# Kernel optimization log

Measured on AMD Instinct MI355X. Metric: run time of the kernel, lower is better.

Reference implementation:

```python
import jax, jax.numpy as jnp
import numpy as np

B, N, D = 2, 2048, 1024
H, HD = 16, 64


def setup_inputs() -> dict:
    key = jax.random.key(0)
    ks = jax.random.split(key, 5)
    return {
        "hidden_states": jax.random.normal(ks[0], (B, N, D), dtype=jnp.float32),
        "W_attn": jax.random.normal(ks[1], (D, 3 * D), dtype=jnp.float32) * (D ** -0.5),
        "b_attn": jax.random.normal(ks[2], (3 * D,), dtype=jnp.float32) * 0.02,
        "W_proj": jax.random.normal(ks[3], (D, D), dtype=jnp.float32) * (D ** -0.5),
        "b_proj": jax.random.normal(ks[4], (D,), dtype=jnp.float32) * 0.02,
    }


def reference(hidden_states, W_attn, b_attn, W_proj, b_proj):
    # QKV projection: [B,N,3D]
    proj = hidden_states @ W_attn + b_attn
    q, k, v = jnp.split(proj, 3, axis=-1)
    # [B,N,H,HD]
    q = q.reshape(B, N, H, HD)
    k = k.reshape(B, N, H, HD)
    v = v.reshape(B, N, H, HD)
    scale = HD ** -0.5
    # naive attention: full [B,H,Nq,Nkv] score matrix
    attn = jnp.einsum("bqhd,bkhd->bhqk", q, k) * scale
    q_pos = jnp.arange(N)
    kv_pos = jnp.arange(N)
    # mask where kv_pos > start_pos + q_pos (start_pos = 0)
    mask = kv_pos[None, :] > q_pos[:, None]  # [Nq, Nkv]
    attn = jnp.where(mask[None, None, :, :], -jnp.inf, attn)
    attn = jax.nn.softmax(attn, axis=-1)
    out = jnp.einsum("bhqk,bkhd->bqhd", attn, v)  # [B,N,H,HD]
    out = out.reshape(B, N, D)
    return out @ W_proj + b_proj
```

## Files before the change

kernel.cpp:

```cpp
#include <hip/hip_runtime.h>
#include <hip/hip_bf16.h>

#define BB 2
#define NN 2048
#define DDIM 1024
#define HH 16
#define HDD 64

typedef __attribute__((ext_vector_type(8))) short bf16x8;
typedef __attribute__((ext_vector_type(4))) short bf16x4;
typedef __attribute__((ext_vector_type(4))) float f32x4;

__device__ inline ushort f2bf(float x) {
  __hip_bfloat16 h = __float2bfloat16(x);
  ushort u;
  __builtin_memcpy(&u, &h, 2);
  return u;
}
__device__ inline float bf2f(ushort u) {
  unsigned v = (unsigned)u << 16;
  float f;
  __builtin_memcpy(&f, &v, 4);
  return f;
}
__device__ inline float exp2_raw(float x) {
  float r;
  asm("v_exp_f32 %0, %1" : "=v"(r) : "v"(x));
  return r;
}

#define GLOAD_LDS16(g, l)                                                              \
  __builtin_amdgcn_global_load_lds((const __attribute__((address_space(1))) void*)(g), \
                                   (__attribute__((address_space(3))) void*)(l), 16, 0, 0)

__global__ __launch_bounds__(256) void cvt_f32_bf16(const float* __restrict__ in,
                                                    ushort* __restrict__ out, int n4) {
  int i = blockIdx.x * 256 + threadIdx.x;
  if (i >= n4) return;
  float4 a = ((const float4*)in)[i];
  ushort4 o;
  o.x = f2bf(a.x); o.y = f2bf(a.y); o.z = f2bf(a.z); o.w = f2bf(a.w);
  ((ushort4*)out)[i] = o;
}

__global__ __launch_bounds__(256) void transpose_cvt(const float* __restrict__ in,
                                                     ushort* __restrict__ out, int R, int C) {
  __shared__ float tile[32][33];
  int bx = blockIdx.x * 32, by = blockIdx.y * 32;
  int tx = threadIdx.x, ty = threadIdx.y;
#pragma unroll
  for (int r = ty; r < 32; r += 8)
    tile[r][tx] = in[(size_t)(by + r) * C + bx + tx];
  __syncthreads();
#pragma unroll
  for (int r = ty; r < 32; r += 8)
    out[(size_t)(bx + r) * R + by + tx] = f2bf(tile[tx][r]);
}

template <int MODE>
__global__ __launch_bounds__(256) void gemm_bt(const ushort* __restrict__ A,
                                               const ushort* __restrict__ Bt,
                                               const float* __restrict__ bias,
                                               void* __restrict__ Cv,
                                               ushort* __restrict__ Vt,
                                               int M, int N, int K) {
  __shared__ ushort As[128 * 32];
  __shared__ ushort Bs[128 * 32];
  const int tid = threadIdx.x;
  const int wid = tid >> 6, lane = tid & 63;
  const int c = lane & 15, g = lane >> 4;
  const int wm = (wid >> 1) * 64, wn = (wid & 1) * 64;
  const int m0 = blockIdx.y * 128, n0 = blockIdx.x * 128;
  f32x4 acc[4][4] = {};
  for (int k0 = 0; k0 < K; k0 += 32) {
    __syncthreads();
#pragma unroll
    for (int it = 0; it < 2; ++it) {
      int G = tid + it * 256;
      int row = G >> 2, sl = G & 3;
      GLOAD_LDS16(A + (size_t)(m0 + row) * K + k0 + sl * 8, &As[G * 8]);
      GLOAD_LDS16(Bt + (size_t)(n0 + row) * K + k0 + sl * 8, &Bs[G * 8]);
    }
    __syncthreads();
    bf16x8 af[4], bfr[4];
#pragma unroll
    for (int i = 0; i < 4; ++i) {
      af[i] = *(const bf16x8*)(&As[(wm + i * 16 + c) * 32 + g * 8]);
      bfr[i] = *(const bf16x8*)(&Bs[(wn + i * 16 + c) * 32 + g * 8]);
    }
#pragma unroll
    for (int i = 0; i < 4; ++i)
#pragma unroll
      for (int j = 0; j < 4; ++j)
        acc[i][j] = __builtin_amdgcn_mfma_f32_16x16x32_bf16(af[i], bfr[j], acc[i][j], 0, 0, 0);
  }
#pragma unroll
  for (int i = 0; i < 4; ++i) {
#pragma unroll
    for (int j = 0; j < 4; ++j) {
      const int col = n0 + wn + j * 16 + c;
      const float bv = bias[col];
      const int row = m0 + wm + i * 16 + g * 4;
      if (MODE == 2 && col >= 2048) {
        const int hh = (col - 2048) >> 6, dd = (col - 2048) & 63;
        const int bb = row >> 11, nl = row & 2047;
        ushort4 ov;
        ov.x = f2bf(acc[i][j][0] + bv);
        ov.y = f2bf(acc[i][j][1] + bv);
        ov.z = f2bf(acc[i][j][2] + bv);
        ov.w = f2bf(acc[i][j][3] + bv);
        *(ushort4*)(&Vt[(size_t)((bb * 16 + hh) * 64 + dd) * NN + nl]) = ov;
      } else {
        const int ldc = (MODE == 2) ? 2048 : N;
#pragma unroll
        for (int ri = 0; ri < 4; ++ri) {
          float v = acc[i][j][ri] + bv;
          ((ushort*)Cv)[(size_t)(row + ri) * ldc + col] = f2bf(v);
        }
      }
    }
  }
}

__global__ __launch_bounds__(256) void gemm_proj(const ushort* __restrict__ A,
                                                 const ushort* __restrict__ Bt,
                                                 const float* __restrict__ bias,
                                                 float* __restrict__ C, int M, int N, int K) {
  __shared__ ushort As[64 * 32];
  __shared__ ushort Bs[128 * 32];
  const int tid = threadIdx.x;
  const int wid = tid >> 6, lane = tid & 63;
  const int c = lane & 15, g = lane >> 4;
  const int wn = wid * 32;
  const int m0 = blockIdx.y * 64, n0 = blockIdx.x * 128;
  f32x4 acc[4][2] = {};
  for (int k0 = 0; k0 < K; k0 += 32) {
    __syncthreads();
#pragma unroll
    for (int it = 0; it < 3; ++it) {
      int G = tid + it * 256;
      if (G < 256) {
        int row = G >> 2, sl = G & 3;
        GLOAD_LDS16(A + (size_t)(m0 + row) * K + k0 + sl * 8, &As[G * 8]);
      } else {
        int GB = G - 256;
        int row = GB >> 2, sl = GB & 3;
        GLOAD_LDS16(Bt + (size_t)(n0 + row) * K + k0 + sl * 8, &Bs[GB * 8]);
      }
    }
    __syncthreads();
    bf16x8 af[4], bfr[2];
#pragma unroll
    for (int i = 0; i < 4; ++i) af[i] = *(const bf16x8*)(&As[(i * 16 + c) * 32 + g * 8]);
#pragma unroll
    for (int j = 0; j < 2; ++j)
      bfr[j] = *(const bf16x8*)(&Bs[(wn + j * 16 + c) * 32 + g * 8]);
#pragma unroll
    for (int i = 0; i < 4; ++i)
#pragma unroll
      for (int j = 0; j < 2; ++j)
        acc[i][j] = __builtin_amdgcn_mfma_f32_16x16x32_bf16(af[i], bfr[j], acc[i][j], 0, 0, 0);
  }
#pragma unroll
  for (int i = 0; i < 4; ++i) {
#pragma unroll
    for (int j = 0; j < 2; ++j) {
      const int col = n0 + wn + j * 16 + c;
      const float bv = bias[col];
      const int row = m0 + i * 16 + g * 4;
#pragma unroll
      for (int ri = 0; ri < 4; ++ri)
        C[(size_t)(row + ri) * N + col] = acc[i][j][ri] + bv;
    }
  }
}

__global__ __launch_bounds__(512) void attn_fwd(const ushort* __restrict__ QK,
                                                const ushort* __restrict__ Vt,
                                                ushort* __restrict__ O) {
  const int bh = blockIdx.x;
  const int b = bh >> 4, h = bh & 15;
  const int qb = (int)gridDim.y - 1 - (int)blockIdx.y;
  const int tid = threadIdx.x;
  const int wid = tid >> 6, lane = tid & 63;
  const int c = lane & 15, g = lane >> 4;
  const int q0 = qb * 128 + wid * 16;
  const ushort* Qb = QK + (size_t)b * NN * 2048 + (size_t)h * HDD;
  const ushort* Kb = Qb + 1024;
  const ushort* Vb = Vt + (size_t)bh * HDD * NN;

  __shared__ ushort Ks[2][64 * 64];
  __shared__ ushort Vs[2][64 * 64];

  const float SC = 0.18033688011112042f;
  bf16x8 qf[2];
  {
    const ushort* qrow = Qb + (size_t)(q0 + c) * 2048 + g * 8;
    qf[0] = *(const bf16x8*)(qrow);
    qf[1] = *(const bf16x8*)(qrow + 32);
#pragma unroll
    for (int r = 0; r < 2; ++r)
#pragma unroll
      for (int e = 0; e < 8; ++e) qf[r][e] = (short)f2bf(bf2f((ushort)qf[r][e]) * SC);
  }

  f32x4 oacc[4] = {};
  float m = 0.f, lsum = 0.f;
  const int q_abs = q0 + c;
  const int tdiag = 2 * qb + (wid >> 2);

#define STAGE_TILE(kv0, bufi)                                                   \
  do {                                                                          \
    int u = tid;                                                                \
    int row = u >> 3, sl = u & 7;                                               \
    int ksl = (sl ^ (row & 7)) * 8;                                             \
    GLOAD_LDS16(Kb + (size_t)((kv0) + row) * 2048 + ksl, &Ks[bufi][u * 8]);     \
    GLOAD_LDS16(Vb + (size_t)row * NN + (kv0) + ksl, &Vs[bufi][u * 8]);         \
  } while (0)

  STAGE_TILE(0, 0);
  __syncthreads();
  int cur = 0;
  const int ntiles = 2 * qb + 2;

  for (int t = 0; t < ntiles; ++t) {
    if (t < ntiles - 1) STAGE_TILE((t + 1) * 64, cur ^ 1);

    if (t <= tdiag) {
      f32x4 s[4] = {};
#pragma unroll
      for (int f = 0; f < 4; ++f) {
        int krow = f * 16 + c;
#pragma unroll
        for (int dc = 0; dc < 2; ++dc) {
          int slot = (dc * 4 + g) ^ (krow & 7);
          bf16x8 kf = *(const bf16x8*)(&Ks[cur][krow * 64 + slot * 8]);
          s[f] = __builtin_amdgcn_mfma_f32_16x16x32_bf16(kf, qf[dc], s[f], 0, 0, 0);
        }
      }

      float pmax = -INFINITY;
      if (t == tdiag) {
        const int kv0 = t * 64;
#pragma unroll
        for (int f = 0; f < 4; ++f)
#pragma unroll
          for (int i = 0; i < 4; ++i) {
            if (kv0 + f * 16 + g * 4 + i > q_abs) s[f][i] = -INFINITY;
            pmax = fmaxf(pmax, s[f][i]);
          }
      } else {
#pragma unroll
        for (int f = 0; f < 4; ++f)
#pragma unroll
          for (int i = 0; i < 4; ++i) pmax = fmaxf(pmax, s[f][i]);
      }

      if (t == 0) {
        float pr = fmaxf(pmax, __shfl_xor(pmax, 16));
        pr = fmaxf(pr, __shfl_xor(pr, 32));
        m = pr;
      } else if (!__all(pmax <= m + 8.f)) {
        float pr = fmaxf(pmax, __shfl_xor(pmax, 16));
        pr = fmaxf(pr, __shfl_xor(pr, 32));
        float mnew = fmaxf(m, pr);
        float corr = exp2_raw(m - mnew);
        lsum *= corr;
#pragma unroll
        for (int db = 0; db < 4; ++db) {
          oacc[db][0] *= corr; oacc[db][1] *= corr;
          oacc[db][2] *= corr; oacc[db][3] *= corr;
        }
        m = mnew;
      }

      float psum = 0.f;
#pragma unroll
      for (int f = 0; f < 4; ++f)
#pragma unroll
        for (int i = 0; i < 4; ++i) {
          float p = exp2_raw(s[f][i] - m);
          s[f][i] = p;
          psum += p;
        }
      lsum += psum;

#pragma unroll
      for (int f = 0; f < 4; ++f) {
        bf16x4 pb;
        pb[0] = (short)f2bf(s[f][0]);
        pb[1] = (short)f2bf(s[f][1]);
        pb[2] = (short)f2bf(s[f][2]);
        pb[3] = (short)f2bf(s[f][3]);
        const int slot = f * 2 + (g >> 1);
#pragma unroll
        for (int db = 0; db < 4; ++db) {
          int d = db * 16 + c;
          bf16x4 vf =
              *(const bf16x4*)(&Vs[cur][d * 64 + ((slot ^ (d & 7)) * 8) + (g & 1) * 4]);
          oacc[db] = __builtin_amdgcn_mfma_f32_16x16x16bf16_1k(vf, pb, oacc[db], 0, 0, 0);
        }
      }
    }
    __syncthreads();
    cur ^= 1;
  }

  lsum += __shfl_xor(lsum, 16);
  lsum += __shfl_xor(lsum, 32);
  float invl = 1.f / lsum;
  ushort* orow = O + (size_t)(b * NN + q0 + c) * DDIM + h * HDD;
#pragma unroll
  for (int db = 0; db < 4; ++db) {
    ushort4 ov;
    ov.x = f2bf(oacc[db][0] * invl);
    ov.y = f2bf(oacc[db][1] * invl);
    ov.z = f2bf(oacc[db][2] * invl);
    ov.w = f2bf(oacc[db][3] * invl);
    *(ushort4*)(&orow[db * 16 + g * 4]) = ov;
  }
}

extern "C" void kernel_launch(void* const* d_in, const int* in_sizes, int n_in,
                              void* d_out, int out_size, void* d_ws, size_t ws_size,
                              hipStream_t stream) {
  const float* hidden = (const float*)d_in[0];
  const float* W_attn = (const float*)d_in[1];
  const float* b_attn = (const float*)d_in[2];
  const float* W_proj = (const float*)d_in[3];
  const float* b_proj = (const float*)d_in[4];

  char* ws = (char*)d_ws;
  ushort* hbf  = (ushort*)(ws);
  ushort* WaT  = (ushort*)(ws + (size_t)(8 << 20));
  ushort* WpT  = (ushort*)(ws + (size_t)(14 << 20));
  ushort* qk   = (ushort*)(ws + (size_t)(16 << 20));
  ushort* vt   = (ushort*)(ws + (size_t)(32 << 20));
  ushort* aout = (ushort*)(ws + (size_t)(40 << 20));

  cvt_f32_bf16<<<4096, 256, 0, stream>>>(hidden, hbf, (BB * NN * DDIM) / 4);
  transpose_cvt<<<dim3(96, 32), dim3(32, 8), 0, stream>>>(W_attn, WaT, 1024, 3072);
  transpose_cvt<<<dim3(32, 32), dim3(32, 8), 0, stream>>>(W_proj, WpT, 1024, 1024);

  gemm_bt<2><<<dim3(24, 32), 256, 0, stream>>>(hbf, WaT, b_attn, qk, vt, 4096, 3072, 1024);
  attn_fwd<<<dim3(32, 16), 512, 0, stream>>>(qk, vt, aout);
  gemm_proj<<<dim3(8, 64), 256, 0, stream>>>(aout, WpT, b_proj, (float*)d_out, 4096, 1024, 1024);
}
```

Baseline: 197.7 us.

## Split long causal query blocks across two workgroups and merge the partial results

The eight longest causal query blocks now have their KV range split in two halves, each handled by a separate workgroup. Each half writes an unnormalized bf16 partial output plus its row max and sum, and a new combine kernel merges the two halves. The point is to balance the triangular workload across more CUs. The three preprocessing kernels are also fused into one launch. In exchange there is an extra kernel launch, partial outputs rounded to bf16 before the merge, and the partials reuse workspace regions that previously held hbf and WaT after those buffers are no longer needed.

```diff
diff --git a/kernel.cpp b/kernel.cpp
--- a/kernel.cpp
+++ b/kernel.cpp
@@ -33,21 +33,39 @@
   __builtin_amdgcn_global_load_lds((const __attribute__((address_space(1))) void*)(g), \
                                    (__attribute__((address_space(3))) void*)(l), 16, 0, 0)
 
-__global__ __launch_bounds__(256) void cvt_f32_bf16(const float* __restrict__ in,
-                                                    ushort* __restrict__ out, int n4) {
-  int i = blockIdx.x * 256 + threadIdx.x;
-  if (i >= n4) return;
-  float4 a = ((const float4*)in)[i];
-  ushort4 o;
-  o.x = f2bf(a.x); o.y = f2bf(a.y); o.z = f2bf(a.z); o.w = f2bf(a.w);
-  ((ushort4*)out)[i] = o;
-}
-
-__global__ __launch_bounds__(256) void transpose_cvt(const float* __restrict__ in,
-                                                     ushort* __restrict__ out, int R, int C) {
+__global__ __launch_bounds__(256) void prep(const float* __restrict__ hidden,
+                                            const float* __restrict__ W_attn,
+                                            const float* __restrict__ W_proj,
+                                            ushort* __restrict__ hbf,
+                                            ushort* __restrict__ WaT,
+                                            ushort* __restrict__ WpT) {
   __shared__ float tile[32][33];
-  int bx = blockIdx.x * 32, by = blockIdx.y * 32;
-  int tx = threadIdx.x, ty = threadIdx.y;
+  const int bid = blockIdx.x, tid = threadIdx.x;
+  if (bid < 2048) {
+    int i = bid * 256 + tid;
+    const float4* in4 = (const float4*)hidden;
+#pragma unroll
+    for (int r = 0; r < 2; ++r, i += 524288) {
+      float4 a = in4[i];
+      ushort4 o;
+      o.x = f2bf(a.x); o.y = f2bf(a.y); o.z = f2bf(a.z); o.w = f2bf(a.w);
+      ((ushort4*)hbf)[i] = o;
+    }
+    return;
+  }
+  const float* in;
+  ushort* out;
+  int R, C, bx, by;
+  if (bid < 2048 + 3072) {
+    int b2 = bid - 2048;
+    in = W_attn; out = WaT; R = 1024; C = 3072;
+    bx = (b2 % 96) * 32; by = (b2 / 96) * 32;
+  } else {
+    int b3 = bid - 2048 - 3072;
+    in = W_proj; out = WpT; R = 1024; C = 1024;
+    bx = (b3 & 31) * 32; by = (b3 >> 5) * 32;
+  }
+  const int tx = tid & 31, ty = tid >> 5;
 #pragma unroll
   for (int r = ty; r < 32; r += 8)
     tile[r][tx] = in[(size_t)(by + r) * C + bx + tx];
@@ -177,10 +195,23 @@
 
 __global__ __launch_bounds__(512) void attn_fwd(const ushort* __restrict__ QK,
                                                 const ushort* __restrict__ Vt,
-                                                ushort* __restrict__ O) {
+                                                ushort* __restrict__ O,
+                                                ushort* __restrict__ partO,
+                                                float* __restrict__ partML) {
   const int bh = blockIdx.x;
   const int b = bh >> 4, h = bh & 15;
-  const int qb = (int)gridDim.y - 1 - (int)blockIdx.y;
+  const int y = blockIdx.y;
+  int qb, t_lo, t_hi, half;
+  bool split;
+  if (y < 8) {
+    qb = y; t_lo = 0; t_hi = 2 * qb + 2; half = 0; split = false;
+  } else {
+    int u = y - 8;
+    qb = 8 + (u >> 1); half = u & 1; split = true;
+    int mid = qb + 1;
+    t_lo = half ? mid : 0;
+    t_hi = half ? (2 * qb + 2) : mid;
+  }
   const int tid = threadIdx.x;
   const int wid = tid >> 6, lane = tid & 63;
   const int c = lane & 15, g = lane >> 4;
@@ -218,13 +249,12 @@
     GLOAD_LDS16(Vb + (size_t)row * NN + (kv0) + ksl, &Vs[bufi][u * 8]);         \
   } while (0)
 
-  STAGE_TILE(0, 0);
+  STAGE_TILE(t_lo * 64, 0);
   __syncthreads();
   int cur = 0;
-  const int ntiles = 2 * qb + 2;
-
-  for (int t = 0; t < ntiles; ++t) {
-    if (t < ntiles - 1) STAGE_TILE((t + 1) * 64, cur ^ 1);
+
+  for (int t = t_lo; t < t_hi; ++t) {
+    if (t + 1 < t_hi) STAGE_TILE((t + 1) * 64, cur ^ 1);
 
     if (t <= tdiag) {
       f32x4 s[4] = {};
@@ -256,7 +286,7 @@
           for (int i = 0; i < 4; ++i) pmax = fmaxf(pmax, s[f][i]);
       }
 
-      if (t == 0) {
+      if (t == t_lo) {
         float pr = fmaxf(pmax, __shfl_xor(pmax, 16));
         pr = fmaxf(pr, __shfl_xor(pr, 32));
         m = pr;
@@ -308,16 +338,65 @@
 
   lsum += __shfl_xor(lsum, 16);
   lsum += __shfl_xor(lsum, 32);
-  float invl = 1.f / lsum;
-  ushort* orow = O + (size_t)(b * NN + q0 + c) * DDIM + h * HDD;
-#pragma unroll
-  for (int db = 0; db < 4; ++db) {
-    ushort4 ov;
-    ov.x = f2bf(oacc[db][0] * invl);
-    ov.y = f2bf(oacc[db][1] * invl);
-    ov.z = f2bf(oacc[db][2] * invl);
-    ov.w = f2bf(oacc[db][3] * invl);
-    *(ushort4*)(&orow[db * 16 + g * 4]) = ov;
+
+  if (!split) {
+    float invl = 1.f / lsum;
+    ushort* orow = O + (size_t)(b * NN + q0 + c) * DDIM + h * HDD;
+#pragma unroll
+    for (int db = 0; db < 4; ++db) {
+      ushort4 ov;
+      ov.x = f2bf(oacc[db][0] * invl);
+      ov.y = f2bf(oacc[db][1] * invl);
+      ov.z = f2bf(oacc[db][2] * invl);
+      ov.w = f2bf(oacc[db][3] * invl);
+      *(ushort4*)(&orow[db * 16 + g * 4]) = ov;
+    }
+  } else {
+    const int e = (((bh << 3) + (qb - 8)) << 1) + half;
+    const int ql = wid * 16 + c;
+    if (g == 0) {
+      partML[(size_t)e * 256 + ql] = m;
+      partML[(size_t)e * 256 + 128 + ql] = lsum;
+    }
+    ushort* po = partO + (size_t)e * 8192 + ql * 64;
+#pragma unroll
+    for (int db = 0; db < 4; ++db) {
+      ushort4 ov;
+      ov.x = f2bf(oacc[db][0]);
+      ov.y = f2bf(oacc[db][1]);
+      ov.z = f2bf(oacc[db][2]);
+      ov.w = f2bf(oacc[db][3]);
+      *(ushort4*)(&po[db * 16 + g * 4]) = ov;
+    }
+  }
+}
+
+__global__ __launch_bounds__(256) void attn_combine(const ushort* __restrict__ partO,
+                                                    const float* __restrict__ partML,
+                                                    ushort* __restrict__ O) {
+  const int bh = blockIdx.x, qb8 = blockIdx.y;
+  const int b = bh >> 4, h = bh & 15;
+  const int tid = threadIdx.x;
+  const int q = tid & 127, dh = tid >> 7;
+  const int e0 = (((bh << 3) + qb8) << 1), e1 = e0 + 1;
+  const float ma = partML[(size_t)e0 * 256 + q], la = partML[(size_t)e0 * 256 + 128 + q];
+  const float mb = partML[(size_t)e1 * 256 + q], lb = partML[(size_t)e1 * 256 + 128 + q];
+  const float mm = fmaxf(ma, mb);
+  const float wa = exp2_raw(ma - mm), wb = exp2_raw(mb - mm);
+  const float inv = 1.f / (la * wa + lb * wb);
+  const ushort* pa = partO + (size_t)e0 * 8192 + q * 64 + dh * 32;
+  const ushort* pc = partO + (size_t)e1 * 8192 + q * 64 + dh * 32;
+  const int qg = (8 + qb8) * 128 + q;
+  ushort* out = O + (size_t)(b * NN + qg) * DDIM + h * HDD + dh * 32;
+#pragma unroll
+  for (int j0 = 0; j0 < 32; j0 += 8) {
+    bf16x8 va = *(const bf16x8*)(pa + j0);
+    bf16x8 vb = *(const bf16x8*)(pc + j0);
+    bf16x8 vo;
+#pragma unroll
+    for (int e = 0; e < 8; ++e)
+      vo[e] = (short)f2bf((bf2f((ushort)va[e]) * wa + bf2f((ushort)vb[e]) * wb) * inv);
+    *(bf16x8*)(out + j0) = vo;
   }
 }
 
@@ -337,12 +416,12 @@
   ushort* qk   = (ushort*)(ws + (size_t)(16 << 20));
   ushort* vt   = (ushort*)(ws + (size_t)(32 << 20));
   ushort* aout = (ushort*)(ws + (size_t)(40 << 20));
-
-  cvt_f32_bf16<<<4096, 256, 0, stream>>>(hidden, hbf, (BB * NN * DDIM) / 4);
-  transpose_cvt<<<dim3(96, 32), dim3(32, 8), 0, stream>>>(W_attn, WaT, 1024, 3072);
-  transpose_cvt<<<dim3(32, 32), dim3(32, 8), 0, stream>>>(W_proj, WpT, 1024, 1024);
-
+  ushort* partO  = (ushort*)(ws);
+  float*  partML = (float*)(ws + (size_t)(8 << 20));
+
+  prep<<<2048 + 3072 + 1024, 256, 0, stream>>>(hidden, W_attn, W_proj, hbf, WaT, WpT);
   gemm_bt<2><<<dim3(24, 32), 256, 0, stream>>>(hbf, WaT, b_attn, qk, vt, 4096, 3072, 1024);
-  attn_fwd<<<dim3(32, 16), 512, 0, stream>>>(qk, vt, aout);
+  attn_fwd<<<dim3(32, 24), 512, 0, stream>>>(qk, vt, aout, partO, partML);
+  attn_combine<<<dim3(32, 8), 256, 0, stream>>>(partO, partML, aout);
   gemm_proj<<<dim3(8, 64), 256, 0, stream>>>(aout, WpT, b_proj, (float*)d_out, 4096, 1024, 1024);
 }
```

Result: faster. 191.6 us (-3.1%).
